# Kernel optimization log

Hardware: AMD Instinct MI355X
Metric: run time of the kernel (lower is better)

Reference implementation:

```python
import jax, jax.numpy as jnp
import numpy as np

E, D, A, EMB, V = 2048, 512, 512, 512, 10000  # encoder_dim, decoder_dim, attention_dim, embed_dim, vocab


def setup_inputs() -> dict:
    key = jax.random.key(0)
    ks = jax.random.split(key, 20)
    s = 0.02
    B, P, T = 64, 196, 40
    return {
        "encoder_out": jax.random.normal(ks[0], (B, P, E), jnp.float32),
        "captions": jax.random.randint(ks[1], (B, T), 0, V),
        "caption_lengths": jax.random.randint(ks[2], (B,), 1, T),
        "enc_att_W": jax.random.normal(ks[3], (E, A)) * s,
        "enc_att_b": jnp.zeros((A,)),
        "dec_att_W": jax.random.normal(ks[4], (D, A)) * s,
        "dec_att_b": jnp.zeros((A,)),
        "full_att_W": jax.random.normal(ks[5], (A,)) * s,
        "full_att_b": jnp.zeros(()),
        "embedding": jax.random.normal(ks[6], (V, EMB)) * s,
        "W_ih": jax.random.normal(ks[7], (EMB + E, 4 * D)) * s,
        "b_ih": jnp.zeros((4 * D,)),
        "W_hh": jax.random.normal(ks[8], (D, 4 * D)) * s,
        "b_hh": jnp.zeros((4 * D,)),
        "init_h_W": jax.random.normal(ks[9], (E, D)) * s,
        "init_h_b": jnp.zeros((D,)),
        "init_c_W": jax.random.normal(ks[10], (E, D)) * s,
        "init_c_b": jnp.zeros((D,)),
        "fc_W": jax.random.normal(ks[11], (D, V)) * s,
        "fc_b": jnp.zeros((V,)),
        "f_beta_W": jax.random.normal(ks[12], (D, E)) * s,
        "f_beta_b": jnp.zeros((E,)),
    }


def reference(encoder_out, captions, caption_lengths,
              enc_att_W, enc_att_b, dec_att_W, dec_att_b, full_att_W, full_att_b,
              embedding, W_ih, b_ih, W_hh, b_hh,
              init_h_W, init_h_b, init_c_W, init_c_b,
              fc_W, fc_b, f_beta_W, f_beta_b):
    # init hidden state from mean-pooled encoder features
    mean_enc = encoder_out.mean(axis=1)                      # [B, E]
    h = mean_enc @ init_h_W + init_h_b                       # [B, D]
    c = mean_enc @ init_c_W + init_c_b

    embs = embedding[captions]                               # [B, T, EMB]
    # encoder_att(encoder_out) is step-invariant -> precompute once
    att1 = jnp.einsum('bpe,ea->bpa', encoder_out, enc_att_W) + enc_att_b  # [B, P, A]

    def step(carry, emb_t):
        h, c = carry
        att2 = h @ dec_att_W + dec_att_b                     # [B, A]
        e = jax.nn.relu(att1 + att2[:, None, :]) @ full_att_W + full_att_b  # [B, P]
        alpha = jax.nn.softmax(e, axis=1)                    # [B, P]
        context = jnp.einsum('bpe,bp->be', encoder_out, alpha)  # [B, E]
        gate = jax.nn.sigmoid(h @ f_beta_W + f_beta_b)       # [B, E]
        x = jnp.concatenate([emb_t, gate * context], axis=1)  # [B, EMB+E]
        gates = x @ W_ih + b_ih + h @ W_hh + b_hh            # [B, 4D]
        i, f, g, o = jnp.split(gates, 4, axis=1)
        c_new = jax.nn.sigmoid(f) * c + jax.nn.sigmoid(i) * jnp.tanh(g)
        h_new = jax.nn.sigmoid(o) * jnp.tanh(c_new)
        preds = h_new @ fc_W + fc_b                          # [B, V] (dropout = identity at eval)
        return (h_new, c_new), (preds, alpha)

    (_, _), (preds_t, alphas_t) = jax.lax.scan(step, (h, c), jnp.swapaxes(embs, 0, 1))
    predictions = jnp.swapaxes(preds_t, 0, 1)                # [B, T, V]
    alphas = jnp.swapaxes(alphas_t, 0, 1)                    # [B, T, P]
    return predictions, alphas
```

## Files before the change

### kernel.cpp

```cpp
#include <hip/hip_runtime.h>
#include <cstdint>
#include <cstddef>

#define B_   64
#define P_   196
#define E_   2048
#define A_   512
#define D_   512
#define EMB_ 512
#define V_   10000
#define T_   40
#define NCAT  14608
#define NCATP 14656

typedef unsigned short u16;
typedef __attribute__((ext_vector_type(8))) short bf16x8;
typedef __attribute__((ext_vector_type(4))) float f32x4;

__device__ __forceinline__ f32x4 mfma_bf16(bf16x8 a, bf16x8 b, f32x4 c) {
  return __builtin_amdgcn_mfma_f32_16x16x32_bf16(a, b, c, 0, 0, 0);
}
__device__ __forceinline__ u16 f2b(float f) {
  unsigned u = __builtin_bit_cast(unsigned, f);
  u += 0x7fffu + ((u >> 16) & 1u);
  return (u16)(u >> 16);
}
__device__ __forceinline__ float b2f(u16 s) {
  unsigned u = ((unsigned)s) << 16;
  return __builtin_bit_cast(float, u);
}
__device__ __forceinline__ float sigf(float x) { return 1.0f / (1.0f + __expf(-x)); }

__device__ __forceinline__ void gl_lds16(const u16* gsrc, u16* ldst) {
  __builtin_amdgcn_global_load_lds(
      (const __attribute__((address_space(1))) unsigned int*)gsrc,
      (__attribute__((address_space(3))) unsigned int*)ldst,
      16, 0, 0);
}

__global__ __launch_bounds__(256) void k_cvt_bf16(const float* __restrict__ s,
                                                  u16* __restrict__ d, int n4) {
  int i = blockIdx.x * 256 + threadIdx.x;
  if (i >= n4) return;
  float4 v = reinterpret_cast<const float4*>(s)[i];
  u16* o = d + (size_t)i * 4;
  o[0] = f2b(v.x); o[1] = f2b(v.y); o[2] = f2b(v.z); o[3] = f2b(v.w);
}

__global__ __launch_bounds__(256) void k_mean(const float* __restrict__ enc,
                                              u16* __restrict__ meanE_bf) {
  int i = blockIdx.x * 256 + threadIdx.x;
  int b = i >> 11, e = i & 2047;
  const float* p = enc + (size_t)b * P_ * E_ + e;
  float s = 0.f;
  for (int pp = 0; pp < P_; ++pp) s += p[(size_t)pp * E_];
  meanE_bf[i] = f2b(s * (1.0f / (float)P_));
}

__global__ __launch_bounds__(256) void k_transpose_bf16(
    const float* __restrict__ src, int srcStride,
    u16* __restrict__ dst, int dstStride, int N, int K) {
  __shared__ float t[32][33];
  int kt = blockIdx.x * 32, nt = blockIdx.y * 32;
  int tx = threadIdx.x & 31, ty = threadIdx.x >> 5;
  #pragma unroll
  for (int i = 0; i < 4; ++i) {
    int k = kt + ty + i * 8, n = nt + tx;
    t[ty + i * 8][tx] = (k < K && n < N) ? src[(size_t)k * srcStride + n] : 0.0f;
  }
  __syncthreads();
  #pragma unroll
  for (int i = 0; i < 4; ++i) {
    int n = nt + ty + i * 8, k = kt + tx;
    if (n < N && k < K) dst[(size_t)n * dstStride + k] = f2b(t[tx][ty + i * 8]);
  }
}

__global__ __launch_bounds__(256) void k_emb(const int* __restrict__ captions,
                                             const float* __restrict__ embedding,
                                             u16* __restrict__ embs) {
  int i = blockIdx.x * 256 + threadIdx.x;
  int m = i >> 9, k = i & 511;
  int t = m >> 6, b = m & 63;
  int cap = captions[b * T_ + t];
  embs[i] = f2b(embedding[(size_t)cap * EMB_ + k]);
}

__global__ __launch_bounds__(256) void k_bsum(const float* __restrict__ a,
                                              const float* __restrict__ b,
                                              float* __restrict__ o) {
  int i = blockIdx.x * 256 + threadIdx.x;
  o[i] = a[i] + b[i];
}

__global__ __launch_bounds__(256) void k_catbias(const float* __restrict__ hb,
                                                 const float* __restrict__ cb,
                                                 float* __restrict__ o) {
  int i = blockIdx.x * 256 + threadIdx.x;
  o[i] = (i < 512) ? hb[i] : cb[i - 512];
}

__global__ __launch_bounds__(256) void k_hc_pack(const float* __restrict__ initHC,
                                                 u16* __restrict__ h_bf,
                                                 float* __restrict__ c_f) {
  int i = blockIdx.x * 256 + threadIdx.x;
  int b = i >> 9, d = i & 511;
  h_bf[i] = f2b(initHC[b * 1024 + d]);
  c_f[i]  = initHC[b * 1024 + 512 + d];
}

template <bool BF16OUT>
__global__ __launch_bounds__(256) void k_gemm_bt(
    const u16* __restrict__ Am, const u16* __restrict__ Bt,
    const float* __restrict__ bias, void* __restrict__ outp, int K, int N) {
  int m0 = blockIdx.x * 64, n0 = blockIdx.y * 64;
  int w = threadIdx.x >> 6, lane = threadIdx.x & 63;
  int lr = lane & 15, lg = lane >> 4;
  const u16* ap = Am + (size_t)(m0 + 16 * w + lr) * K + lg * 8;
  const u16* bp = Bt + (size_t)(n0 + lr) * K + lg * 8;
  f32x4 acc0 = {}, acc1 = {}, acc2 = {}, acc3 = {};
  for (int k = 0; k < K; k += 32) {
    bf16x8 a  = *reinterpret_cast<const bf16x8*>(ap + k);
    bf16x8 b0 = *reinterpret_cast<const bf16x8*>(bp + k);
    bf16x8 b1 = *reinterpret_cast<const bf16x8*>(bp + (size_t)16 * K + k);
    bf16x8 b2 = *reinterpret_cast<const bf16x8*>(bp + (size_t)32 * K + k);
    bf16x8 b3 = *reinterpret_cast<const bf16x8*>(bp + (size_t)48 * K + k);
    acc0 = mfma_bf16(a, b0, acc0);
    acc1 = mfma_bf16(a, b1, acc1);
    acc2 = mfma_bf16(a, b2, acc2);
    acc3 = mfma_bf16(a, b3, acc3);
  }
  int row = m0 + 16 * w + 4 * lg;
  f32x4 accs[4] = {acc0, acc1, acc2, acc3};
  #pragma unroll
  for (int ns = 0; ns < 4; ++ns) {
    int col = n0 + 16 * ns + lr;
    float bv = bias[col];
    #pragma unroll
    for (int r = 0; r < 4; ++r) {
      float v = accs[ns][r] + bv;
      if (BF16OUT) ((u16*)outp)[(size_t)(row + r) * N + col] = f2b(v);
      else         ((float*)outp)[(size_t)(row + r) * N + col] = v;
    }
  }
}

template <bool BF16OUT>
__global__ __launch_bounds__(256) void k_gemm128(
    const u16* __restrict__ Am, const u16* __restrict__ Bt,
    const float* __restrict__ bias, void* __restrict__ outp, int K, int N) {
  __shared__ u16 lA[128 * 64];
  __shared__ u16 lB[128 * 64];
  int n0 = blockIdx.x * 128, m0 = blockIdx.y * 128;
  int w = threadIdx.x >> 6, lane = threadIdx.x & 63;
  int wr = w >> 1, wc = w & 1;
  int lr = lane & 15, lg = lane >> 4;
  int srow = lane >> 3;
  int scol = (lane & 7) * 8;
  f32x4 acc[4][4] = {};
  for (int kt = 0; kt < K; kt += 64) {
    #pragma unroll
    for (int q = 0; q < 4; ++q) {
      int r = (w * 4 + q) * 8 + srow;
      gl_lds16(Am + (size_t)(m0 + r) * K + kt + scol, &lA[(w * 4 + q) * 512]);
      gl_lds16(Bt + (size_t)(n0 + r) * K + kt + scol, &lB[(w * 4 + q) * 512]);
    }
    __syncthreads();
    #pragma unroll
    for (int kk = 0; kk < 2; ++kk) {
      bf16x8 af[4], bf[4];
      #pragma unroll
      for (int m = 0; m < 4; ++m)
        af[m] = *reinterpret_cast<const bf16x8*>(&lA[(wr * 64 + m * 16 + lr) * 64 + kk * 32 + lg * 8]);
      #pragma unroll
      for (int n = 0; n < 4; ++n)
        bf[n] = *reinterpret_cast<const bf16x8*>(&lB[(wc * 64 + n * 16 + lr) * 64 + kk * 32 + lg * 8]);
      #pragma unroll
      for (int m = 0; m < 4; ++m)
        #pragma unroll
        for (int n = 0; n < 4; ++n)
          acc[m][n] = mfma_bf16(af[m], bf[n], acc[m][n]);
    }
    __syncthreads();
  }
  #pragma unroll
  for (int n = 0; n < 4; ++n) {
    int col = n0 + wc * 64 + n * 16 + lr;
    float bv = bias[col];
    #pragma unroll
    for (int m = 0; m < 4; ++m) {
      int row = m0 + wr * 64 + m * 16 + lg * 4;
      #pragma unroll
      for (int r = 0; r < 4; ++r) {
        float v = acc[m][n][r] + bv;
        if (BF16OUT) ((u16*)outp)[(size_t)(row + r) * N + col] = f2b(v);
        else         ((float*)outp)[(size_t)(row + r) * N + col] = v;
      }
    }
  }
}

__global__ __launch_bounds__(256) void k_stepA(
    const u16* __restrict__ h_bf, const u16* __restrict__ catW,
    const float* __restrict__ dec_b, const float* __restrict__ fbeta_b,
    const float* __restrict__ fc_b, const float* __restrict__ embW_t,
    float* __restrict__ att2, float* __restrict__ gate,
    float* __restrict__ gates, float* __restrict__ preds, int wp) {
  int n0 = blockIdx.x * 64;
  int w = threadIdx.x >> 6, lane = threadIdx.x & 63;
  int lr = lane & 15, lg = lane >> 4;
  const u16* ap = h_bf + (size_t)(16 * w + lr) * 512 + lg * 8;
  const u16* bp = catW + (size_t)(n0 + lr) * 512 + lg * 8;
  f32x4 acc0 = {}, acc1 = {}, acc2 = {}, acc3 = {};
  for (int k = 0; k < 512; k += 32) {
    bf16x8 a  = *reinterpret_cast<const bf16x8*>(ap + k);
    bf16x8 b0 = *reinterpret_cast<const bf16x8*>(bp + k);
    bf16x8 b1 = *reinterpret_cast<const bf16x8*>(bp + (size_t)16 * 512 + k);
    bf16x8 b2 = *reinterpret_cast<const bf16x8*>(bp + (size_t)32 * 512 + k);
    bf16x8 b3 = *reinterpret_cast<const bf16x8*>(bp + (size_t)48 * 512 + k);
    acc0 = mfma_bf16(a, b0, acc0);
    acc1 = mfma_bf16(a, b1, acc1);
    acc2 = mfma_bf16(a, b2, acc2);
    acc3 = mfma_bf16(a, b3, acc3);
  }
  int brow = 16 * w + 4 * lg;
  f32x4 accs[4] = {acc0, acc1, acc2, acc3};
  #pragma unroll
  for (int ns = 0; ns < 4; ++ns) {
    int n = n0 + 16 * ns + lr;
    #pragma unroll
    for (int r = 0; r < 4; ++r) {
      int b = brow + r;
      float v = accs[ns][r];
      if (n < 512) {
        att2[b * 512 + n] = v + dec_b[n];
      } else if (n < 2560) {
        int j = n - 512;
        gate[b * 2048 + j] = sigf(v + fbeta_b[j]);
      } else if (n < 4608) {
        int j = n - 2560;
        gates[b * 2048 + j] = v + embW_t[b * 2048 + j];
      } else if (n < 14608) {
        int j = n - 4608;
        if (wp) preds[(size_t)b * (T_ * V_) + j] = v + fc_b[j];
      }
    }
  }
}

__global__ __launch_bounds__(256) void k_stepB(
    const u16* __restrict__ att1, const float* __restrict__ att2,
    const float* __restrict__ wf, const float* __restrict__ bf_,
    float* __restrict__ e) {
  int unit = blockIdx.x * 4 + (threadIdx.x >> 6);
  int lane = threadIdx.x & 63;
  int b = unit / 196;
  const u16*  a1  = att1 + (size_t)unit * 512 + lane * 8;
  const float* a2 = att2 + b * 512 + lane * 8;
  const float* wv = wf + lane * 8;
  float s = 0.f;
  #pragma unroll
  for (int j = 0; j < 8; ++j) {
    float x = b2f(a1[j]) + a2[j];
    s += fmaxf(x, 0.f) * wv[j];
  }
  #pragma unroll
  for (int off = 32; off > 0; off >>= 1) s += __shfl_xor(s, off);
  if (lane == 0) e[unit] = s + bf_[0];
}

__global__ __launch_bounds__(256) void k_stepD(
    const float* __restrict__ e, const u16* __restrict__ enc_bf,
    const float* __restrict__ gate, float* __restrict__ alphas,
    u16* __restrict__ gctx) {
  __shared__ float sal[P_];
  __shared__ float red[256];
  int b = blockIdx.x >> 3, ch = blockIdx.x & 7;
  int tid = threadIdx.x;
  float ev = (tid < P_) ? e[b * P_ + tid] : -1e30f;
  red[tid] = ev; __syncthreads();
  for (int s = 128; s > 0; s >>= 1) {
    if (tid < s) red[tid] = fmaxf(red[tid], red[tid + s]);
    __syncthreads();
  }
  float mx = red[0]; __syncthreads();
  float ex = (tid < P_) ? __expf(ev - mx) : 0.f;
  red[tid] = ex; __syncthreads();
  for (int s = 128; s > 0; s >>= 1) {
    if (tid < s) red[tid] += red[tid + s];
    __syncthreads();
  }
  float inv = 1.0f / red[0];
  if (tid < P_) {
    float al = ex * inv;
    sal[tid] = al;
    if (ch == 0) alphas[(size_t)b * (T_ * P_) + tid] = al;
  }
  __syncthreads();
  int eidx = ch * 256 + tid;
  const u16* ep = enc_bf + (size_t)b * P_ * E_ + eidx;
  float acc = 0.f;
  #pragma unroll 4
  for (int p = 0; p < P_; ++p) acc += sal[p] * b2f(ep[(size_t)p * E_]);
  gctx[b * E_ + eidx] = f2b(acc * gate[b * E_ + eidx]);
}

__global__ __launch_bounds__(256) void k_stepE1(
    const u16* __restrict__ gctx, const u16* __restrict__ Wt,
    float* __restrict__ gates) {
  int n0 = (blockIdx.x & 31) * 64;
  int k0 = (blockIdx.x >> 5) * 256;
  int w = threadIdx.x >> 6, lane = threadIdx.x & 63;
  int lr = lane & 15, lg = lane >> 4;
  const u16* ap = gctx + (size_t)(16 * w + lr) * 2048 + lg * 8 + k0;
  const u16* bp = Wt + (size_t)(n0 + lr) * 2048 + lg * 8 + k0;
  f32x4 acc0 = {}, acc1 = {}, acc2 = {}, acc3 = {};
  for (int k = 0; k < 256; k += 32) {
    bf16x8 a  = *reinterpret_cast<const bf16x8*>(ap + k);
    bf16x8 b0 = *reinterpret_cast<const bf16x8*>(bp + k);
    bf16x8 b1 = *reinterpret_cast<const bf16x8*>(bp + (size_t)16 * 2048 + k);
    bf16x8 b2 = *reinterpret_cast<const bf16x8*>(bp + (size_t)32 * 2048 + k);
    bf16x8 b3 = *reinterpret_cast<const bf16x8*>(bp + (size_t)48 * 2048 + k);
    acc0 = mfma_bf16(a, b0, acc0);
    acc1 = mfma_bf16(a, b1, acc1);
    acc2 = mfma_bf16(a, b2, acc2);
    acc3 = mfma_bf16(a, b3, acc3);
  }
  int brow = 16 * w + 4 * lg;
  f32x4 accs[4] = {acc0, acc1, acc2, acc3};
  #pragma unroll
  for (int ns = 0; ns < 4; ++ns) {
    int n = n0 + 16 * ns + lr;
    #pragma unroll
    for (int r = 0; r < 4; ++r)
      atomicAdd(&gates[(brow + r) * 2048 + n], accs[ns][r]);
  }
}

__global__ __launch_bounds__(256) void k_stepE2(
    const float* __restrict__ gates, float* __restrict__ c, u16* __restrict__ h_bf) {
  int i = blockIdx.x * 256 + threadIdx.x;
  int b = i >> 9, d = i & 511;
  const float* g = gates + (size_t)b * 2048;
  float gi = g[d], gf = g[d + 512], gg = g[d + 1024], go = g[d + 1536];
  float cn = sigf(gf) * c[i] + sigf(gi) * tanhf(gg);
  float hn = sigf(go) * tanhf(cn);
  c[i] = cn;
  h_bf[i] = f2b(hn);
}

extern "C" void kernel_launch(void* const* d_in, const int* in_sizes, int n_in,
                              void* d_out, int out_size, void* d_ws, size_t ws_size,
                              hipStream_t stream) {
  (void)in_sizes; (void)n_in; (void)out_size;
  const float* enc        = (const float*)d_in[0];
  const int*   captions   = (const int*)d_in[1];
  const float* enc_att_W  = (const float*)d_in[3];
  const float* enc_att_b  = (const float*)d_in[4];
  const float* dec_att_W  = (const float*)d_in[5];
  const float* dec_att_b  = (const float*)d_in[6];
  const float* full_att_W = (const float*)d_in[7];
  const float* full_att_b = (const float*)d_in[8];
  const float* embedding  = (const float*)d_in[9];
  const float* W_ih       = (const float*)d_in[10];
  const float* b_ih       = (const float*)d_in[11];
  const float* W_hh       = (const float*)d_in[12];
  const float* b_hh       = (const float*)d_in[13];
  const float* init_h_W   = (const float*)d_in[14];
  const float* init_h_b   = (const float*)d_in[15];
  const float* init_c_W   = (const float*)d_in[16];
  const float* init_c_b   = (const float*)d_in[17];
  const float* fc_W       = (const float*)d_in[18];
  const float* fc_b       = (const float*)d_in[19];
  const float* f_beta_W   = (const float*)d_in[20];
  const float* f_beta_b   = (const float*)d_in[21];

  float* preds_out  = (float*)d_out;
  float* alphas_out = (float*)d_out + (size_t)B_ * T_ * V_;

  char* w = (char*)d_ws;
  auto alloc = [&](size_t bytes) -> char* {
    char* p = w; w += (bytes + 255) & ~(size_t)255; return p;
  };
  u16*   enc_bf   = (u16*)  alloc((size_t)B_ * P_ * E_ * 2);
  u16*   att1_bf  = (u16*)  alloc((size_t)B_ * P_ * A_ * 2);
  u16*   catW     = (u16*)  alloc((size_t)NCATP * 512 * 2);
  u16*   encattWT = (u16*)  alloc((size_t)A_ * E_ * 2);
  u16*   WihembT  = (u16*)  alloc((size_t)2048 * 512 * 2);
  u16*   Wih2T    = (u16*)  alloc((size_t)2048 * 2048 * 2);
  u16*   embs_bf  = (u16*)  alloc((size_t)T_ * B_ * EMB_ * 2);
  float* embW     = (float*)alloc((size_t)(T_ + 1) * B_ * 2048 * 4);
  u16*   catInit  = (u16*)  alloc((size_t)1024 * 2048 * 2);
  float* catInitB = (float*)alloc(1024 * 4);
  float* initHC   = (float*)alloc((size_t)B_ * 1024 * 4);
  u16*   meanE_bf = (u16*)  alloc((size_t)B_ * E_ * 2);
  u16*   h_bf     = (u16*)  alloc((size_t)B_ * D_ * 2);
  float* c_f      = (float*)alloc((size_t)B_ * D_ * 4);
  float* att2_f   = (float*)alloc((size_t)B_ * A_ * 4);
  float* gate_f   = (float*)alloc((size_t)B_ * E_ * 4);
  float* gates_f  = (float*)alloc((size_t)B_ * 2048 * 4);
  float* e_f      = (float*)alloc((size_t)B_ * P_ * 4);
  u16*   gctx_bf  = (u16*)  alloc((size_t)B_ * E_ * 2);
  float* bsum     = (float*)alloc(2048 * 4);
  if ((size_t)(w - (char*)d_ws) > ws_size) return;

  k_cvt_bf16<<<25088, 256, 0, stream>>>(enc, enc_bf, (B_ * P_ * E_) / 4);
  k_mean<<<512, 256, 0, stream>>>(enc, meanE_bf);
  k_transpose_bf16<<<dim3(16, 16), 256, 0, stream>>>(dec_att_W, 512, catW, 512, 512, 512);
  k_transpose_bf16<<<dim3(16, 64), 256, 0, stream>>>(f_beta_W, 2048, catW + (size_t)512 * 512, 512, 2048, 512);
  k_transpose_bf16<<<dim3(16, 64), 256, 0, stream>>>(W_hh, 2048, catW + (size_t)2560 * 512, 512, 2048, 512);
  k_transpose_bf16<<<dim3(16, 313), 256, 0, stream>>>(fc_W, 10000, catW + (size_t)4608 * 512, 512, 10000, 512);
  hipMemsetAsync(catW + (size_t)NCAT * 512, 0, (size_t)(NCATP - NCAT) * 512 * 2, stream);
  k_transpose_bf16<<<dim3(64, 16), 256, 0, stream>>>(enc_att_W, 512, encattWT, 2048, 512, 2048);
  k_transpose_bf16<<<dim3(16, 64), 256, 0, stream>>>(W_ih, 2048, WihembT, 512, 2048, 512);
  k_transpose_bf16<<<dim3(64, 64), 256, 0, stream>>>(W_ih + (size_t)512 * 2048, 2048, Wih2T, 2048, 2048, 2048);
  k_transpose_bf16<<<dim3(64, 16), 256, 0, stream>>>(init_h_W, 512, catInit, 2048, 512, 2048);
  k_transpose_bf16<<<dim3(64, 16), 256, 0, stream>>>(init_c_W, 512, catInit + (size_t)512 * 2048, 2048, 512, 2048);
  k_catbias<<<4, 256, 0, stream>>>(init_h_b, init_c_b, catInitB);
  k_bsum<<<8, 256, 0, stream>>>(b_ih, b_hh, bsum);
  k_emb<<<5120, 256, 0, stream>>>(captions, embedding, embs_bf);
  k_gemm_bt<false><<<dim3(1, 16), 256, 0, stream>>>(meanE_bf, catInit, catInitB, initHC, 2048, 1024);
  k_hc_pack<<<128, 256, 0, stream>>>(initHC, h_bf, c_f);
  k_gemm128<true><<<dim3(4, 98), 256, 0, stream>>>(enc_bf, encattWT, enc_att_b, att1_bf, 2048, 512);
  k_gemm128<false><<<dim3(16, 20), 256, 0, stream>>>(embs_bf, WihembT, bsum, embW, 512, 2048);

  for (int t = 0; t <= T_; ++t) {
    int tm1 = t - 1;
    float* preds = preds_out + (size_t)(tm1 < 0 ? 0 : tm1) * V_;
    k_stepA<<<NCATP / 64, 256, 0, stream>>>(h_bf, catW, dec_att_b, f_beta_b, fc_b,
                                            embW + (size_t)t * B_ * 2048,
                                            att2_f, gate_f, gates_f, preds, tm1 >= 0 ? 1 : 0);
    if (t == T_) break;
    k_stepB<<<3136, 256, 0, stream>>>(att1_bf, att2_f, full_att_W, full_att_b, e_f);
    k_stepD<<<512, 256, 0, stream>>>(e_f, enc_bf, gate_f, alphas_out + (size_t)t * P_, gctx_bf);
    k_stepE1<<<256, 256, 0, stream>>>(gctx_bf, Wih2T, gates_f);
    k_stepE2<<<128, 256, 0, stream>>>(gates_f, c_f, h_bf);
  }
}
```

Baseline: 2.558 ms.

## Hoist vocab projection out of recurrence into one batched GEMM

The per-step fc projection of the hidden state, which was fused into the step-A GEMM over a 14656-column concatenated weight, is removed from the time loop. Every hidden state is now stored in a history buffer, and a single LDS-tiled 128x128 MFMA GEMM over all 2560 rows computes the predictions after the loop. This shrinks the serial per-step GEMM from 229 to 72 column blocks and gives the vocab GEMM much better weight reuse. The extra 41st step-A launch is also dropped. The cost is a larger workspace for the stored hidden states and a strided scatter when writing predictions.

```diff
diff --git a/kernel.cpp b/kernel.cpp
--- a/kernel.cpp
+++ b/kernel.cpp
@@ -10,8 +10,8 @@
 #define EMB_ 512
 #define V_   10000
 #define T_   40
-#define NCAT  14608
-#define NCATP 14656
+#define NCAT  4608
+#define VPAD  10112
 
 typedef unsigned short u16;
 typedef __attribute__((ext_vector_type(8))) short bf16x8;
@@ -101,11 +101,11 @@
 }
 
 __global__ __launch_bounds__(256) void k_hc_pack(const float* __restrict__ initHC,
-                                                 u16* __restrict__ h_bf,
+                                                 u16* __restrict__ h0_bf,
                                                  float* __restrict__ c_f) {
   int i = blockIdx.x * 256 + threadIdx.x;
   int b = i >> 9, d = i & 511;
-  h_bf[i] = f2b(initHC[b * 1024 + d]);
+  h0_bf[i] = f2b(initHC[b * 1024 + d]);
   c_f[i]  = initHC[b * 1024 + 512 + d];
 }
 
@@ -200,12 +200,67 @@
   }
 }
 
+__global__ __launch_bounds__(256) void k_gemm_fc(
+    const u16* __restrict__ Hall1, const u16* __restrict__ fcWT,
+    const float* __restrict__ fc_b, float* __restrict__ preds_out) {
+  __shared__ u16 lA[128 * 64];
+  __shared__ u16 lB[128 * 64];
+  int n0 = blockIdx.x * 128, m0 = blockIdx.y * 128;
+  int w = threadIdx.x >> 6, lane = threadIdx.x & 63;
+  int wr = w >> 1, wc = w & 1;
+  int lr = lane & 15, lg = lane >> 4;
+  int srow = lane >> 3;
+  int scol = (lane & 7) * 8;
+  f32x4 acc[4][4] = {};
+  for (int kt = 0; kt < 512; kt += 64) {
+    #pragma unroll
+    for (int q = 0; q < 4; ++q) {
+      int r = (w * 4 + q) * 8 + srow;
+      gl_lds16(Hall1 + (size_t)(m0 + r) * 512 + kt + scol, &lA[(w * 4 + q) * 512]);
+      gl_lds16(fcWT + (size_t)(n0 + r) * 512 + kt + scol, &lB[(w * 4 + q) * 512]);
+    }
+    __syncthreads();
+    #pragma unroll
+    for (int kk = 0; kk < 2; ++kk) {
+      bf16x8 af[4], bf[4];
+      #pragma unroll
+      for (int m = 0; m < 4; ++m)
+        af[m] = *reinterpret_cast<const bf16x8*>(&lA[(wr * 64 + m * 16 + lr) * 64 + kk * 32 + lg * 8]);
+      #pragma unroll
+      for (int n = 0; n < 4; ++n)
+        bf[n] = *reinterpret_cast<const bf16x8*>(&lB[(wc * 64 + n * 16 + lr) * 64 + kk * 32 + lg * 8]);
+      #pragma unroll
+      for (int m = 0; m < 4; ++m)
+        #pragma unroll
+        for (int n = 0; n < 4; ++n)
+          acc[m][n] = mfma_bf16(af[m], bf[n], acc[m][n]);
+    }
+    __syncthreads();
+  }
+  #pragma unroll
+  for (int n = 0; n < 4; ++n) {
+    int col = n0 + wc * 64 + n * 16 + lr;
+    if (col >= V_) continue;
+    float bv = fc_b[col];
+    #pragma unroll
+    for (int m = 0; m < 4; ++m) {
+      int row = m0 + wr * 64 + m * 16 + lg * 4;
+      #pragma unroll
+      for (int r = 0; r < 4; ++r) {
+        int rr = row + r;
+        int t = rr >> 6, b = rr & 63;
+        preds_out[((size_t)b * T_ + t) * V_ + col] = acc[m][n][r] + bv;
+      }
+    }
+  }
+}
+
 __global__ __launch_bounds__(256) void k_stepA(
     const u16* __restrict__ h_bf, const u16* __restrict__ catW,
     const float* __restrict__ dec_b, const float* __restrict__ fbeta_b,
-    const float* __restrict__ fc_b, const float* __restrict__ embW_t,
+    const float* __restrict__ embW_t,
     float* __restrict__ att2, float* __restrict__ gate,
-    float* __restrict__ gates, float* __restrict__ preds, int wp) {
+    float* __restrict__ gates) {
   int n0 = blockIdx.x * 64;
   int w = threadIdx.x >> 6, lane = threadIdx.x & 63;
   int lr = lane & 15, lg = lane >> 4;
@@ -237,12 +292,9 @@
       } else if (n < 2560) {
         int j = n - 512;
         gate[b * 2048 + j] = sigf(v + fbeta_b[j]);
-      } else if (n < 4608) {
+      } else {
         int j = n - 2560;
         gates[b * 2048 + j] = v + embW_t[b * 2048 + j];
-      } else if (n < 14608) {
-        int j = n - 4608;
-        if (wp) preds[(size_t)b * (T_ * V_) + j] = v + fc_b[j];
       }
     }
   }
@@ -338,7 +390,7 @@
 }
 
 __global__ __launch_bounds__(256) void k_stepE2(
-    const float* __restrict__ gates, float* __restrict__ c, u16* __restrict__ h_bf) {
+    const float* __restrict__ gates, float* __restrict__ c, u16* __restrict__ h_out) {
   int i = blockIdx.x * 256 + threadIdx.x;
   int b = i >> 9, d = i & 511;
   const float* g = gates + (size_t)b * 2048;
@@ -346,7 +398,7 @@
   float cn = sigf(gf) * c[i] + sigf(gi) * tanhf(gg);
   float hn = sigf(go) * tanhf(cn);
   c[i] = cn;
-  h_bf[i] = f2b(hn);
+  h_out[i] = f2b(hn);
 }
 
 extern "C" void kernel_launch(void* const* d_in, const int* in_sizes, int n_in,
@@ -384,17 +436,18 @@
   };
   u16*   enc_bf   = (u16*)  alloc((size_t)B_ * P_ * E_ * 2);
   u16*   att1_bf  = (u16*)  alloc((size_t)B_ * P_ * A_ * 2);
-  u16*   catW     = (u16*)  alloc((size_t)NCATP * 512 * 2);
+  u16*   catW     = (u16*)  alloc((size_t)NCAT * 512 * 2);
+  u16*   fcWT     = (u16*)  alloc((size_t)VPAD * 512 * 2);
   u16*   encattWT = (u16*)  alloc((size_t)A_ * E_ * 2);
   u16*   WihembT  = (u16*)  alloc((size_t)2048 * 512 * 2);
   u16*   Wih2T    = (u16*)  alloc((size_t)2048 * 2048 * 2);
   u16*   embs_bf  = (u16*)  alloc((size_t)T_ * B_ * EMB_ * 2);
-  float* embW     = (float*)alloc((size_t)(T_ + 1) * B_ * 2048 * 4);
+  float* embW     = (float*)alloc((size_t)T_ * B_ * 2048 * 4);
+  u16*   Hall     = (u16*)  alloc((size_t)(T_ + 1) * B_ * D_ * 2);
   u16*   catInit  = (u16*)  alloc((size_t)1024 * 2048 * 2);
   float* catInitB = (float*)alloc(1024 * 4);
   float* initHC   = (float*)alloc((size_t)B_ * 1024 * 4);
   u16*   meanE_bf = (u16*)  alloc((size_t)B_ * E_ * 2);
-  u16*   h_bf     = (u16*)  alloc((size_t)B_ * D_ * 2);
   float* c_f      = (float*)alloc((size_t)B_ * D_ * 4);
   float* att2_f   = (float*)alloc((size_t)B_ * A_ * 4);
   float* gate_f   = (float*)alloc((size_t)B_ * E_ * 4);
@@ -409,8 +462,8 @@
   k_transpose_bf16<<<dim3(16, 16), 256, 0, stream>>>(dec_att_W, 512, catW, 512, 512, 512);
   k_transpose_bf16<<<dim3(16, 64), 256, 0, stream>>>(f_beta_W, 2048, catW + (size_t)512 * 512, 512, 2048, 512);
   k_transpose_bf16<<<dim3(16, 64), 256, 0, stream>>>(W_hh, 2048, catW + (size_t)2560 * 512, 512, 2048, 512);
-  k_transpose_bf16<<<dim3(16, 313), 256, 0, stream>>>(fc_W, 10000, catW + (size_t)4608 * 512, 512, 10000, 512);
-  hipMemsetAsync(catW + (size_t)NCAT * 512, 0, (size_t)(NCATP - NCAT) * 512 * 2, stream);
+  hipMemsetAsync(fcWT + (size_t)V_ * 512, 0, (size_t)(VPAD - V_) * 512 * 2, stream);
+  k_transpose_bf16<<<dim3(16, 313), 256, 0, stream>>>(fc_W, 10000, fcWT, 512, 10000, 512);
   k_transpose_bf16<<<dim3(64, 16), 256, 0, stream>>>(enc_att_W, 512, encattWT, 2048, 512, 2048);
   k_transpose_bf16<<<dim3(16, 64), 256, 0, stream>>>(W_ih, 2048, WihembT, 512, 2048, 512);
   k_transpose_bf16<<<dim3(64, 64), 256, 0, stream>>>(W_ih + (size_t)512 * 2048, 2048, Wih2T, 2048, 2048, 2048);
@@ -420,20 +473,21 @@
   k_bsum<<<8, 256, 0, stream>>>(b_ih, b_hh, bsum);
   k_emb<<<5120, 256, 0, stream>>>(captions, embedding, embs_bf);
   k_gemm_bt<false><<<dim3(1, 16), 256, 0, stream>>>(meanE_bf, catInit, catInitB, initHC, 2048, 1024);
-  k_hc_pack<<<128, 256, 0, stream>>>(initHC, h_bf, c_f);
+  k_hc_pack<<<128, 256, 0, stream>>>(initHC, Hall, c_f);
   k_gemm128<true><<<dim3(4, 98), 256, 0, stream>>>(enc_bf, encattWT, enc_att_b, att1_bf, 2048, 512);
   k_gemm128<false><<<dim3(16, 20), 256, 0, stream>>>(embs_bf, WihembT, bsum, embW, 512, 2048);
 
-  for (int t = 0; t <= T_; ++t) {
-    int tm1 = t - 1;
-    float* preds = preds_out + (size_t)(tm1 < 0 ? 0 : tm1) * V_;
-    k_stepA<<<NCATP / 64, 256, 0, stream>>>(h_bf, catW, dec_att_b, f_beta_b, fc_b,
-                                            embW + (size_t)t * B_ * 2048,
-                                            att2_f, gate_f, gates_f, preds, tm1 >= 0 ? 1 : 0);
-    if (t == T_) break;
+  for (int t = 0; t < T_; ++t) {
+    const u16* h_prev = Hall + (size_t)t * B_ * D_;
+    u16* h_next = Hall + (size_t)(t + 1) * B_ * D_;
+    k_stepA<<<NCAT / 64, 256, 0, stream>>>(h_prev, catW, dec_att_b, f_beta_b,
+                                           embW + (size_t)t * B_ * 2048,
+                                           att2_f, gate_f, gates_f);
     k_stepB<<<3136, 256, 0, stream>>>(att1_bf, att2_f, full_att_W, full_att_b, e_f);
     k_stepD<<<512, 256, 0, stream>>>(e_f, enc_bf, gate_f, alphas_out + (size_t)t * P_, gctx_bf);
     k_stepE1<<<256, 256, 0, stream>>>(gctx_bf, Wih2T, gates_f);
-    k_stepE2<<<128, 256, 0, stream>>>(gates_f, c_f, h_bf);
-  }
-}
+    k_stepE2<<<128, 256, 0, stream>>>(gates_f, c_f, h_next);
+  }
+  k_gemm_fc<<<dim3(VPAD / 128, (T_ * B_) / 128), 256, 0, stream>>>(
+      Hall + (size_t)B_ * D_, fcWT, fc_b, preds_out);
+}
```

After: 2.555 ms. Within noise of the previous version (-0.1%).
